# Optimization experiments

Hardware: AMD Instinct MI355X
Metric: run time of the kernel (lower is better)

## Reference

```python
import jax, jax.numpy as jnp
import numpy as np

HID = 101
IN = 3


def lstm_cell(x, h, c, W_ih, W_hh, b_ih, b_hh):
    # PyTorch LSTMCell gate order: i, f, g, o
    gates = x @ W_ih.T + b_ih + h @ W_hh.T + b_hh  # [B, 4H]
    i, f, g, o = jnp.split(gates, 4, axis=-1)
    i = jax.nn.sigmoid(i)
    f = jax.nn.sigmoid(f)
    g = jnp.tanh(g)
    o = jax.nn.sigmoid(o)
    c_new = f * c + i * g
    h_new = o * jnp.tanh(c_new)
    return h_new, c_new


def setup_inputs() -> dict:
    key = jax.random.key(0)
    ks = jax.random.split(key, 12)
    B, T = 1024, 256
    s1 = 1.0 / np.sqrt(HID)
    u = lambda k, shp: jax.random.uniform(k, shp, jnp.float32, -s1, s1)
    return {
        "input": jax.random.normal(ks[0], (B, T, IN), jnp.float32),
        "W_ih1": u(ks[1], (4 * HID, IN)),
        "W_hh1": u(ks[2], (4 * HID, HID)),
        "b_ih1": u(ks[3], (4 * HID,)),
        "b_hh1": u(ks[4], (4 * HID,)),
        "W_ih2": u(ks[5], (4 * HID, HID)),
        "W_hh2": u(ks[6], (4 * HID, HID)),
        "b_ih2": u(ks[7], (4 * HID,)),
        "b_hh2": u(ks[8], (4 * HID,)),
        "Wl": u(ks[9], (IN, HID)),
        "bl": u(ks[10], (IN,)),
        "future": 32,
    }


def reference(input, W_ih1, W_hh1, b_ih1, b_hh1, W_ih2, W_hh2, b_ih2, b_hh2, Wl, bl, future):
    B = input.shape[0]
    h1 = jnp.zeros((B, HID), input.dtype)
    c1 = jnp.zeros((B, HID), input.dtype)
    h2 = jnp.zeros((B, HID), input.dtype)
    c2 = jnp.zeros((B, HID), input.dtype)

    def step(carry, x_t):
        h1, c1, h2, c2 = carry
        h1, c1 = lstm_cell(x_t, h1, c1, W_ih1, W_hh1, b_ih1, b_hh1)
        h2, c2 = lstm_cell(h1, h2, c2, W_ih2, W_hh2, b_ih2, b_hh2)
        out = h2 @ Wl.T + bl  # [B, 3]
        return (h1, c1, h2, c2), out

    xs = jnp.transpose(input, (1, 0, 2))  # [T, B, 3]
    carry, outs = jax.lax.scan(step, (h1, c1, h2, c2), xs)

    if future > 0:
        last_out = outs[-1]

        def fstep(carry, _):
            h1, c1, h2, c2, out = carry
            h1, c1 = lstm_cell(out, h1, c1, W_ih1, W_hh1, b_ih1, b_hh1)
            h2, c2 = lstm_cell(h1, h2, c2, W_ih2, W_hh2, b_ih2, b_hh2)
            out = h2 @ Wl.T + bl
            return (h1, c1, h2, c2, out), out

        _, fouts = jax.lax.scan(fstep, (*carry, last_out), None, length=future)
        outs = jnp.concatenate([outs, fouts], axis=0)

    return jnp.transpose(outs, (1, 0, 2))  # [B, T+future, 3]
```

## Files before the change

### kernel.cpp

```cpp
#include <hip/hip_runtime.h>
#include <hip/hip_bf16.h>

#define HID 101
#define BATCH 1024
#define RPB 4
#define NBLK 256
#define NTHR 512

#define A1SZ  (7*4*4*512)
#define A2SZ  (7*4*8*512)
#define A2OFF A1SZ
#define AOOFF (A1SZ + A2SZ)
#define AOSZ  (4*512)

typedef _Float16 h8 __attribute__((ext_vector_type(8)));
typedef float f4 __attribute__((ext_vector_type(4)));

__global__ void prep_kernel(const float* __restrict__ W_ih1, const float* __restrict__ W_hh1,
                            const float* __restrict__ b_ih1, const float* __restrict__ b_hh1,
                            const float* __restrict__ W_ih2, const float* __restrict__ W_hh2,
                            const float* __restrict__ b_ih2, const float* __restrict__ b_hh2,
                            const float* __restrict__ Wl, _Float16* __restrict__ wsA) {
    int idx = blockIdx.x * blockDim.x + threadIdx.x;
    int stride = gridDim.x * blockDim.x;
    for (int t = idx; t < A1SZ; t += stride) {
        int i = t & 7, lane = (t >> 3) & 63, kt = (t >> 9) & 3, tau = (t >> 11) & 3, w = t >> 13;
        int k = kt * 32 + ((lane >> 4) & 3) * 8 + i;
        int u = 16 * w + (lane & 15);
        float v = 0.f;
        if (u < HID) {
            int g = tau * HID + u;
            if (k < HID) v = W_hh1[g * HID + k];
            else if (k >= 101 && k <= 103) v = W_ih1[g * 3 + (k - 101)];
            else if (k == 104) v = b_ih1[g] + b_hh1[g];
        }
        wsA[t] = (_Float16)v;
    }
    for (int t = idx; t < A2SZ; t += stride) {
        int i = t & 7, lane = (t >> 3) & 63, kt = (t >> 9) & 7, tau = (t >> 12) & 3, w = t >> 14;
        int k = kt * 32 + ((lane >> 4) & 3) * 8 + i;
        int u = 16 * w + (lane & 15);
        float v = 0.f;
        if (u < HID) {
            int g = tau * HID + u;
            if (k < HID) v = W_ih2[g * HID + k];
            else if (k == 104) v = b_ih2[g] + b_hh2[g];
            else if (k >= 128 && k < 128 + HID) v = W_hh2[g * HID + (k - 128)];
        }
        wsA[A2OFF + t] = (_Float16)v;
    }
    for (int t = idx; t < AOSZ; t += stride) {
        int i = t & 7, lane = (t >> 3) & 63, kt = (t >> 9) & 3;
        int k = kt * 32 + ((lane >> 4) & 3) * 8 + i;
        int j = lane & 15;
        float v = (j < 3 && k < HID) ? Wl[j * HID + k] : 0.f;
        wsA[AOOFF + t] = (_Float16)v;
    }
}

__device__ __forceinline__ float sigm(float z) {
    return __builtin_amdgcn_rcpf(1.f + __expf(-z));
}
__device__ __forceinline__ float tanhf_(float z) {
    return 1.f - 2.f * __builtin_amdgcn_rcpf(__expf(2.f * z) + 1.f);
}

__global__ __launch_bounds__(NTHR, 2) void lstm_kernel(
    const float* __restrict__ input, const _Float16* __restrict__ wsA,
    const float* __restrict__ bl, int T, int steps, float* __restrict__ out)
{
    const int tid = threadIdx.x;
    const int wid = tid >> 6, lane = tid & 63;
    const int q = lane >> 4, col = lane & 15;
    const int r0 = blockIdx.x * RPB;
    const int ostride = steps * 3;

    __shared__ _Float16 Hb[2][2048];
    __shared__ _Float16 K2b[2][2048];
    __shared__ float zw[7][4][4][16];

    h8 A1[4][4];
    h8 A2[4][8];
    if (wid < 7) {
        #pragma unroll
        for (int tau = 0; tau < 4; tau++) {
            #pragma unroll
            for (int kt = 0; kt < 4; kt++)
                A1[tau][kt] = *(const volatile h8*)(
                    wsA + ((size_t)((wid * 4 + tau) * 4 + kt) * 512 + lane * 8));
            #pragma unroll
            for (int kt = 0; kt < 8; kt++)
                A2[tau][kt] = *(const volatile h8*)(
                    wsA + (size_t)A2OFF + ((size_t)((wid * 4 + tau) * 8 + kt) * 512 + lane * 8));
        }
    } else {
        #pragma unroll
        for (int kt = 0; kt < 4; kt++)
            A2[0][kt] = *(const volatile h8*)(
                wsA + (size_t)AOOFF + ((size_t)(kt) * 512 + lane * 8));
    }
    const float bl0 = bl[0], bl1 = bl[1], bl2 = bl[2];

    const int r_ew = lane & 3, ul = lane >> 2;
    const int u = 16 * wid + ul;
    const bool ewv = (wid < 7) && (u < HID);
    const int qfu = (u >> 3) & 3;
    const int hslot = (((u >> 5) * 4 + qfu) * 16 + r_ew) * 8 + (u & 7);
    const int boff = (q * 16 + col) * 8;
    const int xr = lane / 3, xj = lane - 3 * xr;
    const int xoff = (12 * 16 + xr) * 8 + 5 + xj;

    for (int i2 = tid; i2 < 2048; i2 += NTHR) {
        Hb[0][i2] = (_Float16)0.f; Hb[1][i2] = (_Float16)0.f;
        K2b[0][i2] = (_Float16)0.f; K2b[1][i2] = (_Float16)0.f;
    }
    __syncthreads();
    if (tid < 16) {
        Hb[0][(13 * 16 + tid) * 8] = (_Float16)1.0f;
        Hb[1][(13 * 16 + tid) * 8] = (_Float16)1.0f;
    }
    if (tid < 12) {
        int r = tid / 3, j = tid - 3 * (tid / 3);
        Hb[1][(12 * 16 + r) * 8 + 5 + j] = (_Float16)input[(size_t)(r0 + r) * T * 3 + j];
    }
    float c1 = 0.f, c2 = 0.f;
    __syncthreads();

    auto STEP = [&](int t, _Float16* Hrd, _Float16* Hwr, _Float16* K2rd, _Float16* K2wr, bool fut) {
        float xv = 0.f;
        if (fut) {
            if (wid == 7) {
                f4 ao = {0.f, 0.f, 0.f, 0.f};
                #pragma unroll
                for (int kt = 0; kt < 4; kt++) {
                    h8 b = *(const h8*)(K2rd + kt * 512 + boff);
                    ao = __builtin_amdgcn_mfma_f32_16x16x32_f16(A2[0][kt], b, ao, 0, 0, 0);
                }
                if (lane < 4) {
                    float o0 = ao[0] + bl0, o1 = ao[1] + bl1, o2 = ao[2] + bl2;
                    float* op = out + (size_t)(r0 + lane) * ostride + (size_t)(t - 1) * 3;
                    op[0] = o0; op[1] = o1; op[2] = o2;
                    Hrd[(12 * 16 + lane) * 8 + 5] = (_Float16)o0;
                    Hrd[(12 * 16 + lane) * 8 + 6] = (_Float16)o1;
                    Hrd[(12 * 16 + lane) * 8 + 7] = (_Float16)o2;
                }
            }
            __syncthreads();
        }
        if (wid < 7) {
            f4 acc0 = {0.f,0.f,0.f,0.f}, acc1 = acc0, acc2 = acc0, acc3 = acc0;
            #pragma unroll
            for (int kt = 0; kt < 4; kt++) {
                h8 b = *(const h8*)(Hrd + kt * 512 + boff);
                acc0 = __builtin_amdgcn_mfma_f32_16x16x32_f16(A1[0][kt], b, acc0, 0, 0, 0);
                acc1 = __builtin_amdgcn_mfma_f32_16x16x32_f16(A1[1][kt], b, acc1, 0, 0, 0);
                acc2 = __builtin_amdgcn_mfma_f32_16x16x32_f16(A1[2][kt], b, acc2, 0, 0, 0);
                acc3 = __builtin_amdgcn_mfma_f32_16x16x32_f16(A1[3][kt], b, acc3, 0, 0, 0);
            }
            if (col < 4) {
                *(f4*)&zw[wid][0][col][4 * q] = acc0;
                *(f4*)&zw[wid][1][col][4 * q] = acc1;
                *(f4*)&zw[wid][2][col][4 * q] = acc2;
                *(f4*)&zw[wid][3][col][4 * q] = acc3;
            }
            float z0 = zw[wid][0][r_ew][ul], z1 = zw[wid][1][r_ew][ul];
            float z2 = zw[wid][2][r_ew][ul], z3 = zw[wid][3][r_ew][ul];
            float ig = sigm(z0), fg = sigm(z1), gg = tanhf_(z2), og = sigm(z3);
            c1 = fg * c1 + ig * gg;
            float h1v = og * tanhf_(c1);
            if (ewv) Hwr[hslot] = (_Float16)h1v;
        } else {
            if (!fut) {
                if (t > 0) {
                    f4 ao = {0.f, 0.f, 0.f, 0.f};
                    #pragma unroll
                    for (int kt = 0; kt < 4; kt++) {
                        h8 b = *(const h8*)(K2rd + kt * 512 + boff);
                        ao = __builtin_amdgcn_mfma_f32_16x16x32_f16(A2[0][kt], b, ao, 0, 0, 0);
                    }
                    if (lane < 4) {
                        float* op = out + (size_t)(r0 + lane) * ostride + (size_t)(t - 1) * 3;
                        op[0] = ao[0] + bl0; op[1] = ao[1] + bl1; op[2] = ao[2] + bl2;
                    }
                }
                if (t + 1 < T && lane < 12)
                    xv = input[(size_t)(r0 + xr) * T * 3 + (size_t)(t + 1) * 3 + xj];
            }
        }
        __syncthreads();
        if (wid < 7) {
            f4 acc0 = {0.f,0.f,0.f,0.f}, acc1 = acc0, acc2 = acc0, acc3 = acc0;
            #pragma unroll
            for (int kt = 0; kt < 4; kt++) {
                h8 b = *(const h8*)(Hwr + kt * 512 + boff);
                acc0 = __builtin_amdgcn_mfma_f32_16x16x32_f16(A2[0][kt], b, acc0, 0, 0, 0);
                acc1 = __builtin_amdgcn_mfma_f32_16x16x32_f16(A2[1][kt], b, acc1, 0, 0, 0);
                acc2 = __builtin_amdgcn_mfma_f32_16x16x32_f16(A2[2][kt], b, acc2, 0, 0, 0);
                acc3 = __builtin_amdgcn_mfma_f32_16x16x32_f16(A2[3][kt], b, acc3, 0, 0, 0);
            }
            #pragma unroll
            for (int kt = 0; kt < 4; kt++) {
                h8 b = *(const h8*)(K2rd + kt * 512 + boff);
                acc0 = __builtin_amdgcn_mfma_f32_16x16x32_f16(A2[0][kt + 4], b, acc0, 0, 0, 0);
                acc1 = __builtin_amdgcn_mfma_f32_16x16x32_f16(A2[1][kt + 4], b, acc1, 0, 0, 0);
                acc2 = __builtin_amdgcn_mfma_f32_16x16x32_f16(A2[2][kt + 4], b, acc2, 0, 0, 0);
                acc3 = __builtin_amdgcn_mfma_f32_16x16x32_f16(A2[3][kt + 4], b, acc3, 0, 0, 0);
            }
            if (col < 4) {
                *(f4*)&zw[wid][0][col][4 * q] = acc0;
                *(f4*)&zw[wid][1][col][4 * q] = acc1;
                *(f4*)&zw[wid][2][col][4 * q] = acc2;
                *(f4*)&zw[wid][3][col][4 * q] = acc3;
            }
            float z0 = zw[wid][0][r_ew][ul], z1 = zw[wid][1][r_ew][ul];
            float z2 = zw[wid][2][r_ew][ul], z3 = zw[wid][3][r_ew][ul];
            float ig = sigm(z0), fg = sigm(z1), gg = tanhf_(z2), og = sigm(z3);
            c2 = fg * c2 + ig * gg;
            float h2v = og * tanhf_(c2);
            if (ewv) K2wr[hslot] = (_Float16)h2v;
        } else {
            if (!fut && t + 1 < T && lane < 12)
                Hwr[xoff] = (_Float16)xv;
        }
        __syncthreads();
    };

    for (int t = 0; t < T; t += 2) {
        STEP(t,     Hb[1], Hb[0], K2b[1], K2b[0], false);
        STEP(t + 1, Hb[0], Hb[1], K2b[0], K2b[1], false);
    }
    for (int t = T; t < steps; t += 2) {
        STEP(t,     Hb[1], Hb[0], K2b[1], K2b[0], true);
        STEP(t + 1, Hb[0], Hb[1], K2b[0], K2b[1], true);
    }
    if (wid == 7) {
        f4 ao = {0.f, 0.f, 0.f, 0.f};
        #pragma unroll
        for (int kt = 0; kt < 4; kt++) {
            h8 b = *(const h8*)(&K2b[1][0] + kt * 512 + boff);
            ao = __builtin_amdgcn_mfma_f32_16x16x32_f16(A2[0][kt], b, ao, 0, 0, 0);
        }
        if (lane < 4) {
            float* op = out + (size_t)(r0 + lane) * ostride + (size_t)(steps - 1) * 3;
            op[0] = ao[0] + bl0; op[1] = ao[1] + bl1; op[2] = ao[2] + bl2;
        }
    }
}

extern "C" void kernel_launch(void* const* d_in, const int* in_sizes, int n_in,
                              void* d_out, int out_size, void* d_ws, size_t ws_size,
                              hipStream_t stream) {
    const float* input = (const float*)d_in[0];
    const float* W_ih1 = (const float*)d_in[1];
    const float* W_hh1 = (const float*)d_in[2];
    const float* b_ih1 = (const float*)d_in[3];
    const float* b_hh1 = (const float*)d_in[4];
    const float* W_ih2 = (const float*)d_in[5];
    const float* W_hh2 = (const float*)d_in[6];
    const float* b_ih2 = (const float*)d_in[7];
    const float* b_hh2 = (const float*)d_in[8];
    const float* Wl    = (const float*)d_in[9];
    const float* bl    = (const float*)d_in[10];
    int T = in_sizes[0] / (BATCH * 3);
    int steps = out_size / (BATCH * 3);
    _Float16* wsA = (_Float16*)d_ws;

    hipLaunchKernelGGL(prep_kernel, dim3(512), dim3(256), 0, stream,
                       W_ih1, W_hh1, b_ih1, b_hh1, W_ih2, W_hh2, b_ih2, b_hh2, Wl, wsA);
    hipLaunchKernelGGL(lstm_kernel, dim3(NBLK), dim3(NTHR), 0, stream,
                       input, wsA, bl, T, steps, (float*)d_out);
}
```

Before: 488.9 us.

## Pack layer-2 K dimension tighter to cut MFMA k-tiles from 8 to 7

Merges the separate h1 and h2 shared buffers into one contiguous staging buffer, with h2 placed right after the padded h1/x/bias block (offset 112 instead of 128). Layer 2's concatenated K then spans 7 k-tiles instead of 8, so each wave issues 28 MFMAs instead of 32 per step and holds fewer weight registers. The output projection weights are re-indexed to read h2 from its new location. The cost is a more intricate interleaving of the two ping-pong buffers, with h2 written into the buffer being read by layer 1.

New measurement: 472.9 us. 3.3% less time.

```diff
diff --git a/kernel.cpp b/kernel.cpp
--- a/kernel.cpp
+++ b/kernel.cpp
@@ -8,7 +8,7 @@
 #define NTHR 512
 
 #define A1SZ  (7*4*4*512)
-#define A2SZ  (7*4*8*512)
+#define A2SZ  (7*4*7*512)
 #define A2OFF A1SZ
 #define AOOFF (A1SZ + A2SZ)
 #define AOSZ  (4*512)
@@ -37,7 +37,10 @@
         wsA[t] = (_Float16)v;
     }
     for (int t = idx; t < A2SZ; t += stride) {
-        int i = t & 7, lane = (t >> 3) & 63, kt = (t >> 9) & 7, tau = (t >> 12) & 3, w = t >> 14;
+        int i = t & 7, lane = (t >> 3) & 63;
+        int rem = t >> 9;
+        int kt = rem % 7; rem /= 7;
+        int tau = rem & 3, w = rem >> 2;
         int k = kt * 32 + ((lane >> 4) & 3) * 8 + i;
         int u = 16 * w + (lane & 15);
         float v = 0.f;
@@ -45,15 +48,15 @@
             int g = tau * HID + u;
             if (k < HID) v = W_ih2[g * HID + k];
             else if (k == 104) v = b_ih2[g] + b_hh2[g];
-            else if (k >= 128 && k < 128 + HID) v = W_hh2[g * HID + (k - 128)];
+            else if (k >= 112 && k < 213) v = W_hh2[g * HID + (k - 112)];
         }
         wsA[A2OFF + t] = (_Float16)v;
     }
     for (int t = idx; t < AOSZ; t += stride) {
-        int i = t & 7, lane = (t >> 3) & 63, kt = (t >> 9) & 3;
-        int k = kt * 32 + ((lane >> 4) & 3) * 8 + i;
+        int i = t & 7, lane = (t >> 3) & 63, kk = (t >> 9) & 3;
+        int k = (kk + 3) * 32 + ((lane >> 4) & 3) * 8 + i;
         int j = lane & 15;
-        float v = (j < 3 && k < HID) ? Wl[j * HID + k] : 0.f;
+        float v = (j < 3 && k >= 112 && k < 213) ? Wl[j * HID + (k - 112)] : 0.f;
         wsA[AOOFF + t] = (_Float16)v;
     }
 }
@@ -75,12 +78,11 @@
     const int r0 = blockIdx.x * RPB;
     const int ostride = steps * 3;
 
-    __shared__ _Float16 Hb[2][2048];
-    __shared__ _Float16 K2b[2][2048];
+    __shared__ _Float16 Sb[2][3584];
     __shared__ float zw[7][4][4][16];
 
     h8 A1[4][4];
-    h8 A2[4][8];
+    h8 A2[4][7];
     if (wid < 7) {
         #pragma unroll
         for (int tau = 0; tau < 4; tau++) {
@@ -89,9 +91,9 @@
                 A1[tau][kt] = *(const volatile h8*)(
                     wsA + ((size_t)((wid * 4 + tau) * 4 + kt) * 512 + lane * 8));
             #pragma unroll
-            for (int kt = 0; kt < 8; kt++)
+            for (int kt = 0; kt < 7; kt++)
                 A2[tau][kt] = *(const volatile h8*)(
-                    wsA + (size_t)A2OFF + ((size_t)((wid * 4 + tau) * 8 + kt) * 512 + lane * 8));
+                    wsA + (size_t)A2OFF + ((size_t)((wid * 4 + tau) * 7 + kt) * 512 + lane * 8));
         }
     } else {
         #pragma unroll
@@ -104,45 +106,44 @@
     const int r_ew = lane & 3, ul = lane >> 2;
     const int u = 16 * wid + ul;
     const bool ewv = (wid < 7) && (u < HID);
-    const int qfu = (u >> 3) & 3;
-    const int hslot = (((u >> 5) * 4 + qfu) * 16 + r_ew) * 8 + (u & 7);
+    const int hs1 = (u >> 3) * 128 + r_ew * 8 + (u & 7);
+    const int hs2 = (14 + (u >> 3)) * 128 + r_ew * 8 + (u & 7);
     const int boff = (q * 16 + col) * 8;
     const int xr = lane / 3, xj = lane - 3 * xr;
-    const int xoff = (12 * 16 + xr) * 8 + 5 + xj;
-
-    for (int i2 = tid; i2 < 2048; i2 += NTHR) {
-        Hb[0][i2] = (_Float16)0.f; Hb[1][i2] = (_Float16)0.f;
-        K2b[0][i2] = (_Float16)0.f; K2b[1][i2] = (_Float16)0.f;
+    const int xoff = 12 * 128 + xr * 8 + 5 + xj;
+
+    for (int i2 = tid; i2 < 3584; i2 += NTHR) {
+        Sb[0][i2] = (_Float16)0.f; Sb[1][i2] = (_Float16)0.f;
     }
     __syncthreads();
     if (tid < 16) {
-        Hb[0][(13 * 16 + tid) * 8] = (_Float16)1.0f;
-        Hb[1][(13 * 16 + tid) * 8] = (_Float16)1.0f;
+        Sb[0][13 * 128 + tid * 8] = (_Float16)1.0f;
+        Sb[1][13 * 128 + tid * 8] = (_Float16)1.0f;
     }
     if (tid < 12) {
         int r = tid / 3, j = tid - 3 * (tid / 3);
-        Hb[1][(12 * 16 + r) * 8 + 5 + j] = (_Float16)input[(size_t)(r0 + r) * T * 3 + j];
+        Sb[1][12 * 128 + r * 8 + 5 + j] = (_Float16)input[(size_t)(r0 + r) * T * 3 + j];
     }
     float c1 = 0.f, c2 = 0.f;
     __syncthreads();
 
-    auto STEP = [&](int t, _Float16* Hrd, _Float16* Hwr, _Float16* K2rd, _Float16* K2wr, bool fut) {
+    auto STEP = [&](int t, _Float16* R, _Float16* W, bool fut) {
         float xv = 0.f;
         if (fut) {
             if (wid == 7) {
                 f4 ao = {0.f, 0.f, 0.f, 0.f};
                 #pragma unroll
-                for (int kt = 0; kt < 4; kt++) {
-                    h8 b = *(const h8*)(K2rd + kt * 512 + boff);
-                    ao = __builtin_amdgcn_mfma_f32_16x16x32_f16(A2[0][kt], b, ao, 0, 0, 0);
+                for (int kk = 0; kk < 4; kk++) {
+                    h8 b = *(const h8*)(W + (kk + 3) * 512 + boff);
+                    ao = __builtin_amdgcn_mfma_f32_16x16x32_f16(A2[0][kk], b, ao, 0, 0, 0);
                 }
                 if (lane < 4) {
                     float o0 = ao[0] + bl0, o1 = ao[1] + bl1, o2 = ao[2] + bl2;
                     float* op = out + (size_t)(r0 + lane) * ostride + (size_t)(t - 1) * 3;
                     op[0] = o0; op[1] = o1; op[2] = o2;
-                    Hrd[(12 * 16 + lane) * 8 + 5] = (_Float16)o0;
-                    Hrd[(12 * 16 + lane) * 8 + 6] = (_Float16)o1;
-                    Hrd[(12 * 16 + lane) * 8 + 7] = (_Float16)o2;
+                    R[12 * 128 + lane * 8 + 5] = (_Float16)o0;
+                    R[12 * 128 + lane * 8 + 6] = (_Float16)o1;
+                    R[12 * 128 + lane * 8 + 7] = (_Float16)o2;
                 }
             }
             __syncthreads();
@@ -151,7 +152,7 @@
             f4 acc0 = {0.f,0.f,0.f,0.f}, acc1 = acc0, acc2 = acc0, acc3 = acc0;
             #pragma unroll
             for (int kt = 0; kt < 4; kt++) {
-                h8 b = *(const h8*)(Hrd + kt * 512 + boff);
+                h8 b = *(const h8*)(R + kt * 512 + boff);
                 acc0 = __builtin_amdgcn_mfma_f32_16x16x32_f16(A1[0][kt], b, acc0, 0, 0, 0);
                 acc1 = __builtin_amdgcn_mfma_f32_16x16x32_f16(A1[1][kt], b, acc1, 0, 0, 0);
                 acc2 = __builtin_amdgcn_mfma_f32_16x16x32_f16(A1[2][kt], b, acc2, 0, 0, 0);
@@ -168,15 +169,15 @@
             float ig = sigm(z0), fg = sigm(z1), gg = tanhf_(z2), og = sigm(z3);
             c1 = fg * c1 + ig * gg;
             float h1v = og * tanhf_(c1);
-            if (ewv) Hwr[hslot] = (_Float16)h1v;
+            if (ewv) W[hs1] = (_Float16)h1v;
         } else {
             if (!fut) {
                 if (t > 0) {
                     f4 ao = {0.f, 0.f, 0.f, 0.f};
                     #pragma unroll
-                    for (int kt = 0; kt < 4; kt++) {
-                        h8 b = *(const h8*)(K2rd + kt * 512 + boff);
-                        ao = __builtin_amdgcn_mfma_f32_16x16x32_f16(A2[0][kt], b, ao, 0, 0, 0);
+                    for (int kk = 0; kk < 4; kk++) {
+                        h8 b = *(const h8*)(W + (kk + 3) * 512 + boff);
+                        ao = __builtin_amdgcn_mfma_f32_16x16x32_f16(A2[0][kk], b, ao, 0, 0, 0);
                     }
                     if (lane < 4) {
                         float* op = out + (size_t)(r0 + lane) * ostride + (size_t)(t - 1) * 3;
@@ -191,20 +192,12 @@
         if (wid < 7) {
             f4 acc0 = {0.f,0.f,0.f,0.f}, acc1 = acc0, acc2 = acc0, acc3 = acc0;
             #pragma unroll
-            for (int kt = 0; kt < 4; kt++) {
-                h8 b = *(const h8*)(Hwr + kt * 512 + boff);
+            for (int kt = 0; kt < 7; kt++) {
+                h8 b = *(const h8*)(W + kt * 512 + boff);
                 acc0 = __builtin_amdgcn_mfma_f32_16x16x32_f16(A2[0][kt], b, acc0, 0, 0, 0);
                 acc1 = __builtin_amdgcn_mfma_f32_16x16x32_f16(A2[1][kt], b, acc1, 0, 0, 0);
                 acc2 = __builtin_amdgcn_mfma_f32_16x16x32_f16(A2[2][kt], b, acc2, 0, 0, 0);
                 acc3 = __builtin_amdgcn_mfma_f32_16x16x32_f16(A2[3][kt], b, acc3, 0, 0, 0);
-            }
-            #pragma unroll
-            for (int kt = 0; kt < 4; kt++) {
-                h8 b = *(const h8*)(K2rd + kt * 512 + boff);
-                acc0 = __builtin_amdgcn_mfma_f32_16x16x32_f16(A2[0][kt + 4], b, acc0, 0, 0, 0);
-                acc1 = __builtin_amdgcn_mfma_f32_16x16x32_f16(A2[1][kt + 4], b, acc1, 0, 0, 0);
-                acc2 = __builtin_amdgcn_mfma_f32_16x16x32_f16(A2[2][kt + 4], b, acc2, 0, 0, 0);
-                acc3 = __builtin_amdgcn_mfma_f32_16x16x32_f16(A2[3][kt + 4], b, acc3, 0, 0, 0);
             }
             if (col < 4) {
                 *(f4*)&zw[wid][0][col][4 * q] = acc0;
@@ -217,28 +210,28 @@
             float ig = sigm(z0), fg = sigm(z1), gg = tanhf_(z2), og = sigm(z3);
             c2 = fg * c2 + ig * gg;
             float h2v = og * tanhf_(c2);
-            if (ewv) K2wr[hslot] = (_Float16)h2v;
+            if (ewv) R[hs2] = (_Float16)h2v;
         } else {
             if (!fut && t + 1 < T && lane < 12)
-                Hwr[xoff] = (_Float16)xv;
+                W[xoff] = (_Float16)xv;
         }
         __syncthreads();
     };
 
     for (int t = 0; t < T; t += 2) {
-        STEP(t,     Hb[1], Hb[0], K2b[1], K2b[0], false);
-        STEP(t + 1, Hb[0], Hb[1], K2b[0], K2b[1], false);
+        STEP(t,     Sb[1], Sb[0], false);
+        STEP(t + 1, Sb[0], Sb[1], false);
     }
     for (int t = T; t < steps; t += 2) {
-        STEP(t,     Hb[1], Hb[0], K2b[1], K2b[0], true);
-        STEP(t + 1, Hb[0], Hb[1], K2b[0], K2b[1], true);
+        STEP(t,     Sb[1], Sb[0], true);
+        STEP(t + 1, Sb[0], Sb[1], true);
     }
     if (wid == 7) {
         f4 ao = {0.f, 0.f, 0.f, 0.f};
         #pragma unroll
-        for (int kt = 0; kt < 4; kt++) {
-            h8 b = *(const h8*)(&K2b[1][0] + kt * 512 + boff);
-            ao = __builtin_amdgcn_mfma_f32_16x16x32_f16(A2[0][kt], b, ao, 0, 0, 0);
+        for (int kk = 0; kk < 4; kk++) {
+            h8 b = *(const h8*)(&Sb[0][0] + (kk + 3) * 512 + boff);
+            ao = __builtin_amdgcn_mfma_f32_16x16x32_f16(A2[0][kk], b, ao, 0, 0, 0);
         }
         if (lane < 4) {
             float* op = out + (size_t)(r0 + lane) * ostride + (size_t)(steps - 1) * 3;
```
